# Kernel optimization log

Hardware: AMD Instinct MI355X
Metric: run time of the kernel (lower is better)

The kernel has to match this reference:

```python
import jax, jax.numpy as jnp
import numpy as np

B, T, C = 4, 2048, 768
H, D = 6, 128


def apply_rotary_emb(x, cos, sin):
    # x: (B, T, H, D); cos, sin: (1, T, 1, D//2)
    d = x.shape[-1] // 2
    x1, x2 = x[..., :d], x[..., d:]
    y1 = x1 * cos + x2 * sin
    y2 = -x1 * sin + x2 * cos
    return jnp.concatenate([y1, y2], axis=-1)


def rmsnorm(x):
    eps = 1e-15
    ms = jnp.mean(x * x, axis=-1, keepdims=True)
    return x / jnp.sqrt(ms + eps)


def setup_inputs() -> dict:
    key = jax.random.key(0)
    ks = jax.random.split(key, 7)
    s = 0.02
    return {
        "x": jax.random.normal(ks[0], (B, T, C), jnp.float32),
        "cos": jax.random.normal(ks[1], (1, T, 1, D // 2), jnp.float32),
        "sin": jax.random.normal(ks[2], (1, T, 1, D // 2), jnp.float32),
        "Wq": jax.random.normal(ks[3], (C, C), jnp.float32) * s,
        "Wk": jax.random.normal(ks[4], (C, C), jnp.float32) * s,
        "Wv": jax.random.normal(ks[5], (C, C), jnp.float32) * s,
        "Wo": jax.random.normal(ks[6], (C, C), jnp.float32) * s,
    }


def reference(x, cos, sin, Wq, Wk, Wv, Wo):
    b, t, c = x.shape
    # QKV projections (nn.Linear: x @ W.T)
    q = (x @ Wq.T).reshape(b, t, H, D)
    k = (x @ Wk.T).reshape(b, t, H, D)
    v = (x @ Wv.T).reshape(b, t, H, D)
    # RoPE then QK-RMSNorm
    q = rmsnorm(apply_rotary_emb(q, cos, sin))
    k = rmsnorm(apply_rotary_emb(k, cos, sin))
    # (B, H, T, D)
    q = q.transpose(0, 2, 1, 3)
    k = k.transpose(0, 2, 1, 3)
    v = v.transpose(0, 2, 1, 3)
    scores = jnp.einsum('bhqd,bhkd->bhqk', q, k) / jnp.sqrt(jnp.float32(D))
    causal = jnp.tril(jnp.ones((t, t), dtype=bool))
    scores = jnp.where(causal[None, None], scores, -jnp.inf)
    attn = jax.nn.softmax(scores, axis=-1)
    out = jnp.einsum('bhqk,bhkd->bhqd', attn, v)
    out = out.transpose(0, 2, 1, 3).reshape(b, t, c)
    return out @ Wo.T
```

## Files before the change

kernel.cpp:

```cpp
#include <hip/hip_runtime.h>

#define T_SEQ 2048
#define NH    6
#define HD    128
#define CDIM  768
#define NQKV  2304
#define MROWS 8192
#define NSLOT 384
#define QSCL  0.12754011021989615f

typedef __attribute__((ext_vector_type(8)))  short bf16x8;
typedef __attribute__((ext_vector_type(4)))  float f32x4;
typedef __attribute__((ext_vector_type(16))) float f32x16;
typedef __attribute__((ext_vector_type(2)))  int   i32x2;

__device__ __forceinline__ unsigned short f2bf(float f){
  unsigned int u = __builtin_bit_cast(unsigned int, f);
  u += 0x7fffu + ((u >> 16) & 1u);
  return (unsigned short)(u >> 16);
}
__device__ __forceinline__ float bf2f(unsigned short h){
  unsigned int u = ((unsigned int)h) << 16;
  return __builtin_bit_cast(float, u);
}
__device__ __forceinline__ float ex2(float x){
  return __builtin_amdgcn_exp2f(x);
}
__device__ __forceinline__ unsigned int cvtpk(float lo, float hi){
  unsigned int r;
  asm("v_cvt_pk_bf16_f32 %0, %1, %2" : "=v"(r) : "v"(lo), "v"(hi));
  return r;
}

__device__ __forceinline__ void gload_lds16(const void* g, void* l){
  __builtin_amdgcn_global_load_lds(
      (const __attribute__((address_space(1))) unsigned int*)g,
      (__attribute__((address_space(3))) unsigned int*)l, 16, 0, 0);
}

__device__ __forceinline__ int ncq(int Q){
  return Q < 8 ? 1 : 2;
}
__device__ __forceinline__ int cumc(int Q){
  return Q < 8 ? Q : 8 + 2*(Q-8);
}

__global__ __launch_bounds__(256) void cvt_all(
    const float* __restrict__ x,
    const float* __restrict__ w0, const float* __restrict__ w1,
    const float* __restrict__ w2, const float* __restrict__ w3,
    unsigned short* __restrict__ xb, unsigned short* __restrict__ wout){
  const int bid = blockIdx.x;
  const float* src;
  unsigned short* dst;
  int i;
  if (bid < 6144){
    src = x; dst = xb;
    i = bid * 256 + threadIdx.x;
  } else {
    const int wb = bid - 6144;
    const int which = wb / 576;
    src = which == 0 ? w0 : which == 1 ? w1 : which == 2 ? w2 : w3;
    dst = wout + (size_t)which * CDIM * CDIM;
    i = (wb % 576) * 256 + threadIdx.x;
  }
  float4 v = reinterpret_cast<const float4*>(src)[i];
  ushort4 o;
  o.x = f2bf(v.x); o.y = f2bf(v.y); o.z = f2bf(v.z); o.w = f2bf(v.w);
  reinterpret_cast<ushort4*>(dst)[i] = o;
}

template<int EPI>
__global__ __launch_bounds__(256) void gemm_bt(
    const unsigned short* __restrict__ A,
    const unsigned short* __restrict__ B,
    void* __restrict__ Cv, int M, int N, int K,
    const float* __restrict__ cosp, const float* __restrict__ sinp,
    unsigned short* __restrict__ Vt)
{
  __shared__ unsigned short sh[128 * 128];
  unsigned short* As = sh;
  unsigned short* Bs = sh + 128 * 64;
  const int tid  = threadIdx.x;
  const int lane = tid & 63;
  const int wave = tid >> 6;
  const int lr = lane & 15, lg = lane >> 4;
  const int srow = lane >> 3;
  const int sslot = (lane & 7) ^ (lane >> 3);
  const int gx = gridDim.x, gy = gridDim.y, nwg = gx * gy;
  const int flat = blockIdx.y * gx + blockIdx.x;
  const int nf = (flat & 7) * (nwg >> 3) + (flat >> 3);
  const int row0 = (nf / gy) * 128, col0 = (nf % gy) * 128;
  const int wrow = wave * 32;

  f32x4 acc[2][8];
  const f32x4 z = {0.f, 0.f, 0.f, 0.f};
  #pragma unroll
  for (int i = 0; i < 2; ++i)
    #pragma unroll
    for (int j = 0; j < 8; ++j) acc[i][j] = z;

  for (int k0 = 0; k0 < K; k0 += 64){
    #pragma unroll
    for (int i = 0; i < 4; ++i){
      int seg = wave * 4 + i;
      int r = seg * 8 + srow;
      gload_lds16(&A[(size_t)(row0 + r) * K + k0 + sslot * 8], &As[seg * 512]);
      gload_lds16(&B[(size_t)(col0 + r) * K + k0 + sslot * 8], &Bs[seg * 512]);
    }
    __syncthreads();
    #pragma unroll
    for (int kk = 0; kk < 64; kk += 32){
      bf16x8 af[2], bfr[8];
      #pragma unroll
      for (int mi = 0; mi < 2; ++mi)
        af[mi] = *reinterpret_cast<const bf16x8*>(
            &As[(wrow + mi*16 + lr) * 64 + ((((kk>>3) + lg) ^ (lr & 7)) * 8)]);
      #pragma unroll
      for (int ni = 0; ni < 8; ++ni)
        bfr[ni] = *reinterpret_cast<const bf16x8*>(
            &Bs[(ni*16 + lr) * 64 + ((((kk>>3) + lg) ^ (lr & 7)) * 8)]);
      #pragma unroll
      for (int mi = 0; mi < 2; ++mi)
        #pragma unroll
        for (int ni = 0; ni < 8; ++ni)
          acc[mi][ni] = __builtin_amdgcn_mfma_f32_16x16x32_bf16(af[mi], bfr[ni], acc[mi][ni], 0, 0, 0);
    }
    __syncthreads();
  }

  if (EPI == 0){
    float* Cf = reinterpret_cast<float*>(Cv);
    #pragma unroll
    for (int mi = 0; mi < 2; ++mi)
      #pragma unroll
      for (int ni = 0; ni < 8; ++ni)
        #pragma unroll
        for (int r = 0; r < 4; ++r)
          Cf[(size_t)(row0 + wrow + mi*16 + lg*4 + r) * N + col0 + ni*16 + lr] = acc[mi][ni][r];
  } else {
    unsigned short* Cb = reinterpret_cast<unsigned short*>(Cv);
    const int ct = col0 >> 7;
    if (ct >= 12){
      const int hh = ct - 12;
      const int b2 = row0 >> 11, t0 = row0 & (T_SEQ - 1);
      #pragma unroll
      for (int mi = 0; mi < 2; ++mi)
        #pragma unroll
        for (int ni = 0; ni < 8; ++ni)
          #pragma unroll
          for (int r = 0; r < 4; ++r){
            const int trow = wrow + mi*16 + lg*4 + r;
            const int col  = ni*16 + lr;
            sh[trow * 128 + (col ^ ((trow & 7) << 4))] = f2bf(acc[mi][ni][r]);
          }
      __syncthreads();
      const int dd = tid >> 1, tq = (tid & 1) * 64;
      unsigned short* dst =
          Vt + ((size_t)(b2 * NH + hh) * HD + dd) * T_SEQ + t0 + tq;
      #pragma unroll
      for (int j8 = 0; j8 < 8; ++j8){
        union { int4 v; unsigned short u[8]; } w;
        #pragma unroll
        for (int jj = 0; jj < 8; ++jj){
          const int tt = tq + j8 * 8 + jj;
          w.u[jj] = sh[tt * 128 + (dd ^ (jj << 4))];
        }
        *reinterpret_cast<int4*>(&dst[j8 * 8]) = w.v;
      }
    } else {
      const float post = (ct < 6) ? QSCL : 1.0f;
      #pragma unroll
      for (int mi = 0; mi < 2; ++mi){
        #pragma unroll
        for (int r = 0; r < 4; ++r){
          const int row = row0 + wrow + mi*16 + lg*4 + r;
          const int t = row & (T_SEQ - 1);
          float y1[4], y2[4], ssp = 0.f;
          #pragma unroll
          for (int ni = 0; ni < 4; ++ni){
            const int d = ni*16 + lr;
            float c = cosp[t * 64 + d];
            float s = sinp[t * 64 + d];
            float x1 = acc[mi][ni][r], x2 = acc[mi][ni+4][r];
            y1[ni] = x1 * c + x2 * s;
            y2[ni] = x2 * c - x1 * s;
            ssp += y1[ni]*y1[ni] + y2[ni]*y2[ni];
          }
          #pragma unroll
          for (int off = 1; off < 16; off <<= 1) ssp += __shfl_xor(ssp, off);
          const float inv = rsqrtf(ssp * (1.0f / 128.0f) + 1e-15f) * post;
          #pragma unroll
          for (int ni = 0; ni < 4; ++ni){
            const int d = ni*16 + lr;
            Cb[(size_t)row * N + col0 + d]      = f2bf(y1[ni] * inv);
            Cb[(size_t)row * N + col0 + d + 64] = f2bf(y2[ni] * inv);
          }
        }
      }
    }
  }
}

__global__ __launch_bounds__(256) void attn_fwd(
    const unsigned short* __restrict__ QKVb,
    const unsigned short* __restrict__ Vt,
    unsigned short* __restrict__ AO,
    unsigned short* __restrict__ Op, float* __restrict__ Mp, float* __restrict__ Lp)
{
  __shared__ unsigned short Ks[64][136];
  __shared__ unsigned short Vs[128][72];
  const int tid = threadIdx.x;
  const int lane = tid & 63, wave = tid >> 6;
  const int l31 = lane & 31, hi = lane >> 5;

  const int flat = blockIdx.x;
  const int nf = (flat & 7) * 72 + (flat >> 3);
  const int bh = nf / 24;
  const int L = 23 - (nf % 24);
  int Q, c;
  if (L < 8){ Q = L; c = 0; }
  else      { int m = L - 8; Q = 8 + (m >> 1); c = m & 1; }
  const int nc = ncq(Q);
  const int tiles = 2 * Q + 2;
  const int half = tiles >> 1;
  const int tbeg = (nc == 1) ? 0    : c * half;
  const int tend = (nc == 1) ? tiles : tbeg + half;
  const int b = bh / NH, h = bh % NH;
  const int qw = Q * 128 + wave * 32;

  const unsigned short* Qp = QKVb + (size_t)(b * T_SEQ) * NQKV + h * HD;
  const unsigned short* Kp = QKVb + (size_t)(b * T_SEQ) * NQKV + CDIM + h * HD;
  const unsigned short* Vp = Vt + (size_t)bh * HD * T_SEQ;

  const int kr = tid >> 4, kc4 = (tid & 15) * 8;
  const int vr = tid >> 3, vc4 = (tid & 7) * 8;

  bf16x8 qf[8];
  #pragma unroll
  for (int c4 = 0; c4 < 8; ++c4)
    qf[c4] = *reinterpret_cast<const bf16x8*>(
        &Qp[(size_t)(qw + l31) * NQKV + c4 * 16 + hi * 8]);

  f32x16 o[4];
  #pragma unroll
  for (int db = 0; db < 4; ++db)
    #pragma unroll
    for (int r = 0; r < 16; ++r) o[db][r] = 0.f;
  float mrun = -__builtin_inff(), lrun = 0.f;

  int4 gk0, gk1, gk2, gk3, gv0, gv1, gv2, gv3;
  {
    const int kv0 = tbeg * 64;
    gk0 = *reinterpret_cast<const int4*>(&Kp[(size_t)(kv0 + kr)       * NQKV + kc4]);
    gk1 = *reinterpret_cast<const int4*>(&Kp[(size_t)(kv0 + kr + 16)  * NQKV + kc4]);
    gk2 = *reinterpret_cast<const int4*>(&Kp[(size_t)(kv0 + kr + 32)  * NQKV + kc4]);
    gk3 = *reinterpret_cast<const int4*>(&Kp[(size_t)(kv0 + kr + 48)  * NQKV + kc4]);
    gv0 = *reinterpret_cast<const int4*>(&Vp[(size_t)(vr)       * T_SEQ + kv0 + vc4]);
    gv1 = *reinterpret_cast<const int4*>(&Vp[(size_t)(vr + 32)  * T_SEQ + kv0 + vc4]);
    gv2 = *reinterpret_cast<const int4*>(&Vp[(size_t)(vr + 64)  * T_SEQ + kv0 + vc4]);
    gv3 = *reinterpret_cast<const int4*>(&Vp[(size_t)(vr + 96)  * T_SEQ + kv0 + vc4]);
  }

  for (int t = tbeg; t < tend; ++t){
    *reinterpret_cast<int4*>(&Ks[kr][kc4])        = gk0;
    *reinterpret_cast<int4*>(&Ks[kr + 16][kc4])   = gk1;
    *reinterpret_cast<int4*>(&Ks[kr + 32][kc4])   = gk2;
    *reinterpret_cast<int4*>(&Ks[kr + 48][kc4])   = gk3;
    *reinterpret_cast<int4*>(&Vs[vr][vc4])        = gv0;
    *reinterpret_cast<int4*>(&Vs[vr + 32][vc4])   = gv1;
    *reinterpret_cast<int4*>(&Vs[vr + 64][vc4])   = gv2;
    *reinterpret_cast<int4*>(&Vs[vr + 96][vc4])   = gv3;
    __syncthreads();

    if (t + 1 < tend){
      const int kn = (t + 1) * 64;
      gk0 = *reinterpret_cast<const int4*>(&Kp[(size_t)(kn + kr)       * NQKV + kc4]);
      gk1 = *reinterpret_cast<const int4*>(&Kp[(size_t)(kn + kr + 16)  * NQKV + kc4]);
      gk2 = *reinterpret_cast<const int4*>(&Kp[(size_t)(kn + kr + 32)  * NQKV + kc4]);
      gk3 = *reinterpret_cast<const int4*>(&Kp[(size_t)(kn + kr + 48)  * NQKV + kc4]);
      gv0 = *reinterpret_cast<const int4*>(&Vp[(size_t)(vr)       * T_SEQ + kn + vc4]);
      gv1 = *reinterpret_cast<const int4*>(&Vp[(size_t)(vr + 32)  * T_SEQ + kn + vc4]);
      gv2 = *reinterpret_cast<const int4*>(&Vp[(size_t)(vr + 64)  * T_SEQ + kn + vc4]);
      gv3 = *reinterpret_cast<const int4*>(&Vp[(size_t)(vr + 96)  * T_SEQ + kn + vc4]);
    }

    const int kv0 = t * 64;
    if (kv0 <= qw + 31){
      f32x16 s[2];
      #pragma unroll
      for (int r = 0; r < 16; ++r){ s[0][r] = 0.f; s[1][r] = 0.f; }
      __builtin_amdgcn_s_setprio(1);
      #pragma unroll
      for (int c4 = 0; c4 < 8; ++c4){
        bf16x8 k0 = *reinterpret_cast<const bf16x8*>(&Ks[l31][c4 * 16 + hi * 8]);
        bf16x8 k1 = *reinterpret_cast<const bf16x8*>(&Ks[32 + l31][c4 * 16 + hi * 8]);
        s[0] = __builtin_amdgcn_mfma_f32_32x32x16_bf16(k0, qf[c4], s[0], 0, 0, 0);
        s[1] = __builtin_amdgcn_mfma_f32_32x32x16_bf16(k1, qf[c4], s[1], 0, 0, 0);
      }
      __builtin_amdgcn_s_setprio(0);

      const int qg = qw + l31;
      if (kv0 + 63 > qw){
        #pragma unroll
        for (int blk = 0; blk < 2; ++blk)
          #pragma unroll
          for (int r = 0; r < 16; ++r){
            int kg = kv0 + 32 * blk + (r & 3) + 8 * (r >> 2) + 4 * hi;
            s[blk][r] = (kg <= qg) ? s[blk][r] : -__builtin_inff();
          }
      }

      float t8[8];
      #pragma unroll
      for (int blk = 0; blk < 2; ++blk)
        #pragma unroll
        for (int j = 0; j < 4; ++j)
          t8[blk * 4 + j] = fmaxf(fmaxf(s[blk][4*j], s[blk][4*j+1]),
                                  fmaxf(s[blk][4*j+2], s[blk][4*j+3]));
      float pm = fmaxf(fmaxf(fmaxf(t8[0], t8[1]), fmaxf(t8[2], t8[3])),
                       fmaxf(fmaxf(t8[4], t8[5]), fmaxf(t8[6], t8[7])));
      pm = fmaxf(pm, __shfl_xor(pm, 32));

      if (__any(pm > mrun)){
        float mn = fmaxf(mrun, pm);
        float scf = (mrun == -__builtin_inff()) ? 0.f : ex2(mrun - mn);
        mrun = mn; lrun *= scf;
        #pragma unroll
        for (int r = 0; r < 16; ++r){
          float scr = __shfl(scf, (r & 3) + 8 * (r >> 2) + 4 * hi, 32);
          #pragma unroll
          for (int db = 0; db < 4; ++db) o[db][r] *= scr;
        }
      }

      float a8[8];
      #pragma unroll
      for (int blk = 0; blk < 2; ++blk)
        #pragma unroll
        for (int j = 0; j < 4; ++j){
          float p0 = ex2(s[blk][4*j]   - mrun);
          float p1 = ex2(s[blk][4*j+1] - mrun);
          float p2 = ex2(s[blk][4*j+2] - mrun);
          float p3 = ex2(s[blk][4*j+3] - mrun);
          s[blk][4*j] = p0; s[blk][4*j+1] = p1; s[blk][4*j+2] = p2; s[blk][4*j+3] = p3;
          a8[blk * 4 + j] = (p0 + p1) + (p2 + p3);
        }
      float ls = ((a8[0] + a8[1]) + (a8[2] + a8[3])) + ((a8[4] + a8[5]) + (a8[6] + a8[7]));
      lrun += ls + __shfl_xor(ls, 32);

      __builtin_amdgcn_s_setprio(1);
      #pragma unroll
      for (int kc = 0; kc < 4; ++kc){
        const int blk = kc >> 1, base2 = (kc & 1) * 8;
        unsigned int a0 = cvtpk(s[blk][base2+0], s[blk][base2+1]);
        unsigned int b0 = cvtpk(s[blk][base2+4], s[blk][base2+5]);
        unsigned int a1 = cvtpk(s[blk][base2+2], s[blk][base2+3]);
        unsigned int b1 = cvtpk(s[blk][base2+6], s[blk][base2+7]);
        i32x2 sw0 = __builtin_amdgcn_permlane32_swap((int)a0, (int)b0, false, false);
        i32x2 sw1 = __builtin_amdgcn_permlane32_swap((int)a1, (int)b1, false, false);
        union { bf16x8 v; unsigned int u[4]; } pa;
        pa.u[0] = (unsigned int)sw0[0];
        pa.u[1] = (unsigned int)sw1[0];
        pa.u[2] = (unsigned int)sw0[1];
        pa.u[3] = (unsigned int)sw1[1];
        #pragma unroll
        for (int db = 0; db < 4; ++db){
          bf16x8 vf = *reinterpret_cast<const bf16x8*>(
              &Vs[db * 32 + l31][kc * 16 + hi * 8]);
          o[db] = __builtin_amdgcn_mfma_f32_32x32x16_bf16(pa.v, vf, o[db], 0, 0, 0);
        }
      }
      __builtin_amdgcn_s_setprio(0);
    }
    __syncthreads();
  }

  if (nc == 1){
    float inv = 1.0f / lrun;
    #pragma unroll
    for (int r = 0; r < 16; ++r){
      const int crow = (r & 3) + 8 * (r >> 2) + 4 * hi;
      float ir = __shfl(inv, crow, 32);
      #pragma unroll
      for (int db = 0; db < 4; ++db)
        AO[((size_t)b * T_SEQ + qw + crow) * CDIM + h * HD + db * 32 + l31] =
            f2bf(o[db][r] * ir);
    }
  } else {
    const int slot = bh * 16 + 2 * (Q - 8) + c;
    unsigned short* OpW = Op + (size_t)slot * 128 * 128;
    #pragma unroll
    for (int r = 0; r < 16; ++r){
      const int row = wave * 32 + (r & 3) + 8 * (r >> 2) + 4 * hi;
      #pragma unroll
      for (int db = 0; db < 4; ++db)
        OpW[row * 128 + db * 32 + l31] = f2bf(o[db][r]);
    }
    if (hi == 0){
      Mp[(size_t)slot * 128 + wave * 32 + l31] = mrun;
      Lp[(size_t)slot * 128 + wave * 32 + l31] = lrun;
    }
  }
}

__global__ __launch_bounds__(256) void attn_combine(
    const unsigned short* __restrict__ Op, const float* __restrict__ Mp,
    const float* __restrict__ Lp, unsigned short* __restrict__ AO)
{
  const int Q  = 8 + blockIdx.x;
  const int bh = blockIdx.y;
  const int b = bh / NH, h = bh % NH;
  const int slot0 = bh * 16 + 2 * (Q - 8);
  #pragma unroll
  for (int u = 0; u < 16; ++u){
    int unit = threadIdx.x + u * 256;
    int r = unit >> 5, d4 = unit & 31;
    const float m0 = Mp[(size_t)slot0 * 128 + r];
    const float m1 = Mp[(size_t)(slot0 + 1) * 128 + r];
    const float m = fmaxf(m0, m1);
    const float w0 = __builtin_amdgcn_exp2f(m0 - m);
    const float w1 = __builtin_amdgcn_exp2f(m1 - m);
    const float l = w0 * Lp[(size_t)slot0 * 128 + r]
                  + w1 * Lp[(size_t)(slot0 + 1) * 128 + r];
    const ushort4 v0 = *reinterpret_cast<const ushort4*>(
        &Op[((size_t)slot0 * 128 + r) * 128 + d4 * 4]);
    const ushort4 v1 = *reinterpret_cast<const ushort4*>(
        &Op[((size_t)(slot0 + 1) * 128 + r) * 128 + d4 * 4]);
    const float inv = 1.0f / l;
    ushort4 ov;
    ov.x = f2bf((w0 * bf2f(v0.x) + w1 * bf2f(v1.x)) * inv);
    ov.y = f2bf((w0 * bf2f(v0.y) + w1 * bf2f(v1.y)) * inv);
    ov.z = f2bf((w0 * bf2f(v0.z) + w1 * bf2f(v1.z)) * inv);
    ov.w = f2bf((w0 * bf2f(v0.w) + w1 * bf2f(v1.w)) * inv);
    *reinterpret_cast<ushort4*>(
        &AO[((size_t)b * T_SEQ + Q * 128 + r) * CDIM + h * HD + d4 * 4]) = ov;
  }
}

extern "C" void kernel_launch(void* const* d_in, const int* in_sizes, int n_in,
                              void* d_out, int out_size, void* d_ws, size_t ws_size,
                              hipStream_t stream)
{
  (void)in_sizes; (void)n_in; (void)out_size; (void)ws_size;
  const float* x    = (const float*)d_in[0];
  const float* cosp = (const float*)d_in[1];
  const float* sinp = (const float*)d_in[2];
  const float* Wq   = (const float*)d_in[3];
  const float* Wk   = (const float*)d_in[4];
  const float* Wv   = (const float*)d_in[5];
  const float* Wo   = (const float*)d_in[6];
  float* out = (float*)d_out;

  unsigned short* xb    = (unsigned short*)d_ws;
  unsigned short* Wqkvb = xb    + (size_t)MROWS * CDIM;
  unsigned short* Wob   = Wqkvb + (size_t)NQKV * CDIM;
  unsigned short* QKVb  = Wob   + (size_t)CDIM * CDIM;
  unsigned short* Vtb   = QKVb  + (size_t)MROWS * NQKV;
  unsigned short* AO    = Vtb   + (size_t)MROWS * CDIM;
  unsigned short* Op    = AO    + (size_t)MROWS * CDIM;
  float* Mp = (float*)(Op + (size_t)NSLOT * 128 * 128);
  float* Lp = Mp + (size_t)NSLOT * 128;

  cvt_all<<<8448, 256, 0, stream>>>(x, Wq, Wk, Wv, Wo, xb, Wqkvb);

  gemm_bt<1><<<dim3(MROWS / 128, NQKV / 128), 256, 0, stream>>>(
      xb, Wqkvb, QKVb, MROWS, NQKV, CDIM, cosp, sinp, Vtb);
  attn_fwd<<<576, 256, 0, stream>>>(QKVb, Vtb, AO, Op, Mp, Lp);
  attn_combine<<<dim3(8, 24), 256, 0, stream>>>(Op, Mp, Lp, AO);
  gemm_bt<0><<<dim3(MROWS / 128, CDIM / 128), 256, 0, stream>>>(
      AO, Wob, out, MROWS, CDIM, CDIM, nullptr, nullptr, nullptr);
}
```

Before: 176.8 us.

## Stage 128-key K/V tiles per barrier in attention with dynamic LDS

The attention kernel now loads and stages two 64-key K/V tiles (128 keys) into dynamic shared memory per iteration and processes both sub-tiles between barriers. The aim is to halve the number of __syncthreads and global-load rounds per key range and to issue more loads in flight. The split-kernel boundary is moved to an even tile index so each half holds whole 128-key pairs. In exchange LDS use grows to about 68 KB per block and twice as many prefetch registers are live, which may lower occupancy.

```diff
diff --git a/kernel.cpp b/kernel.cpp
--- a/kernel.cpp
+++ b/kernel.cpp
@@ -40,9 +40,6 @@
 
 __device__ __forceinline__ int ncq(int Q){
   return Q < 8 ? 1 : 2;
-}
-__device__ __forceinline__ int cumc(int Q){
-  return Q < 8 ? Q : 8 + 2*(Q-8);
 }
 
 __global__ __launch_bounds__(256) void cvt_all(
@@ -208,8 +205,9 @@
     unsigned short* __restrict__ AO,
     unsigned short* __restrict__ Op, float* __restrict__ Mp, float* __restrict__ Lp)
 {
-  __shared__ unsigned short Ks[64][136];
-  __shared__ unsigned short Vs[128][72];
+  extern __shared__ unsigned short shm[];
+  unsigned short* Ks = shm;
+  unsigned short* Vs = shm + 128 * 136;
   const int tid = threadIdx.x;
   const int lane = tid & 63, wave = tid >> 6;
   const int l31 = lane & 31, hi = lane >> 5;
@@ -223,9 +221,13 @@
   else      { int m = L - 8; Q = 8 + (m >> 1); c = m & 1; }
   const int nc = ncq(Q);
   const int tiles = 2 * Q + 2;
-  const int half = tiles >> 1;
-  const int tbeg = (nc == 1) ? 0    : c * half;
-  const int tend = (nc == 1) ? tiles : tbeg + half;
+  int tbeg, tend;
+  if (nc == 1){ tbeg = 0; tend = tiles; }
+  else {
+    const int half0 = ((Q + 2) >> 1) << 1;
+    tbeg = c ? half0 : 0;
+    tend = c ? tiles : half0;
+  }
   const int b = bh / NH, h = bh % NH;
   const int qw = Q * 128 + wave * 32;
 
@@ -249,52 +251,67 @@
     for (int r = 0; r < 16; ++r) o[db][r] = 0.f;
   float mrun = -__builtin_inff(), lrun = 0.f;
 
-  int4 gk0, gk1, gk2, gk3, gv0, gv1, gv2, gv3;
-  {
-    const int kv0 = tbeg * 64;
-    gk0 = *reinterpret_cast<const int4*>(&Kp[(size_t)(kv0 + kr)       * NQKV + kc4]);
-    gk1 = *reinterpret_cast<const int4*>(&Kp[(size_t)(kv0 + kr + 16)  * NQKV + kc4]);
-    gk2 = *reinterpret_cast<const int4*>(&Kp[(size_t)(kv0 + kr + 32)  * NQKV + kc4]);
-    gk3 = *reinterpret_cast<const int4*>(&Kp[(size_t)(kv0 + kr + 48)  * NQKV + kc4]);
-    gv0 = *reinterpret_cast<const int4*>(&Vp[(size_t)(vr)       * T_SEQ + kv0 + vc4]);
-    gv1 = *reinterpret_cast<const int4*>(&Vp[(size_t)(vr + 32)  * T_SEQ + kv0 + vc4]);
-    gv2 = *reinterpret_cast<const int4*>(&Vp[(size_t)(vr + 64)  * T_SEQ + kv0 + vc4]);
-    gv3 = *reinterpret_cast<const int4*>(&Vp[(size_t)(vr + 96)  * T_SEQ + kv0 + vc4]);
-  }
-
-  for (int t = tbeg; t < tend; ++t){
-    *reinterpret_cast<int4*>(&Ks[kr][kc4])        = gk0;
-    *reinterpret_cast<int4*>(&Ks[kr + 16][kc4])   = gk1;
-    *reinterpret_cast<int4*>(&Ks[kr + 32][kc4])   = gk2;
-    *reinterpret_cast<int4*>(&Ks[kr + 48][kc4])   = gk3;
-    *reinterpret_cast<int4*>(&Vs[vr][vc4])        = gv0;
-    *reinterpret_cast<int4*>(&Vs[vr + 32][vc4])   = gv1;
-    *reinterpret_cast<int4*>(&Vs[vr + 64][vc4])   = gv2;
-    *reinterpret_cast<int4*>(&Vs[vr + 96][vc4])   = gv3;
+  int4 gk0, gk1, gk2, gk3, gk4, gk5, gk6, gk7;
+  int4 gv0, gv1, gv2, gv3, gv4, gv5, gv6, gv7;
+
+#define LOADST(KV0)                                                            \
+  { const int _k = (KV0);                                                      \
+    gk0 = *reinterpret_cast<const int4*>(&Kp[(size_t)(_k + kr)        * NQKV + kc4]); \
+    gk1 = *reinterpret_cast<const int4*>(&Kp[(size_t)(_k + kr + 16)   * NQKV + kc4]); \
+    gk2 = *reinterpret_cast<const int4*>(&Kp[(size_t)(_k + kr + 32)   * NQKV + kc4]); \
+    gk3 = *reinterpret_cast<const int4*>(&Kp[(size_t)(_k + kr + 48)   * NQKV + kc4]); \
+    gk4 = *reinterpret_cast<const int4*>(&Kp[(size_t)(_k + kr + 64)   * NQKV + kc4]); \
+    gk5 = *reinterpret_cast<const int4*>(&Kp[(size_t)(_k + kr + 80)   * NQKV + kc4]); \
+    gk6 = *reinterpret_cast<const int4*>(&Kp[(size_t)(_k + kr + 96)   * NQKV + kc4]); \
+    gk7 = *reinterpret_cast<const int4*>(&Kp[(size_t)(_k + kr + 112)  * NQKV + kc4]); \
+    gv0 = *reinterpret_cast<const int4*>(&Vp[(size_t)(vr)       * T_SEQ + _k + vc4]);      \
+    gv1 = *reinterpret_cast<const int4*>(&Vp[(size_t)(vr + 32)  * T_SEQ + _k + vc4]);      \
+    gv2 = *reinterpret_cast<const int4*>(&Vp[(size_t)(vr + 64)  * T_SEQ + _k + vc4]);      \
+    gv3 = *reinterpret_cast<const int4*>(&Vp[(size_t)(vr + 96)  * T_SEQ + _k + vc4]);      \
+    gv4 = *reinterpret_cast<const int4*>(&Vp[(size_t)(vr)       * T_SEQ + _k + 64 + vc4]); \
+    gv5 = *reinterpret_cast<const int4*>(&Vp[(size_t)(vr + 32)  * T_SEQ + _k + 64 + vc4]); \
+    gv6 = *reinterpret_cast<const int4*>(&Vp[(size_t)(vr + 64)  * T_SEQ + _k + 64 + vc4]); \
+    gv7 = *reinterpret_cast<const int4*>(&Vp[(size_t)(vr + 96)  * T_SEQ + _k + 64 + vc4]); }
+
+  LOADST(tbeg * 64);
+
+  for (int t = tbeg; t < tend; t += 2){
+    *reinterpret_cast<int4*>(&Ks[(kr)       * 136 + kc4]) = gk0;
+    *reinterpret_cast<int4*>(&Ks[(kr + 16)  * 136 + kc4]) = gk1;
+    *reinterpret_cast<int4*>(&Ks[(kr + 32)  * 136 + kc4]) = gk2;
+    *reinterpret_cast<int4*>(&Ks[(kr + 48)  * 136 + kc4]) = gk3;
+    *reinterpret_cast<int4*>(&Ks[(kr + 64)  * 136 + kc4]) = gk4;
+    *reinterpret_cast<int4*>(&Ks[(kr + 80)  * 136 + kc4]) = gk5;
+    *reinterpret_cast<int4*>(&Ks[(kr + 96)  * 136 + kc4]) = gk6;
+    *reinterpret_cast<int4*>(&Ks[(kr + 112) * 136 + kc4]) = gk7;
+    *reinterpret_cast<int4*>(&Vs[(vr)      * 136 + vc4])      = gv0;
+    *reinterpret_cast<int4*>(&Vs[(vr + 32) * 136 + vc4])      = gv1;
+    *reinterpret_cast<int4*>(&Vs[(vr + 64) * 136 + vc4])      = gv2;
+    *reinterpret_cast<int4*>(&Vs[(vr + 96) * 136 + vc4])      = gv3;
+    *reinterpret_cast<int4*>(&Vs[(vr)      * 136 + 64 + vc4]) = gv4;
+    *reinterpret_cast<int4*>(&Vs[(vr + 32) * 136 + 64 + vc4]) = gv5;
+    *reinterpret_cast<int4*>(&Vs[(vr + 64) * 136 + 64 + vc4]) = gv6;
+    *reinterpret_cast<int4*>(&Vs[(vr + 96) * 136 + 64 + vc4]) = gv7;
     __syncthreads();
 
-    if (t + 1 < tend){
-      const int kn = (t + 1) * 64;
-      gk0 = *reinterpret_cast<const int4*>(&Kp[(size_t)(kn + kr)       * NQKV + kc4]);
-      gk1 = *reinterpret_cast<const int4*>(&Kp[(size_t)(kn + kr + 16)  * NQKV + kc4]);
-      gk2 = *reinterpret_cast<const int4*>(&Kp[(size_t)(kn + kr + 32)  * NQKV + kc4]);
-      gk3 = *reinterpret_cast<const int4*>(&Kp[(size_t)(kn + kr + 48)  * NQKV + kc4]);
-      gv0 = *reinterpret_cast<const int4*>(&Vp[(size_t)(vr)       * T_SEQ + kn + vc4]);
-      gv1 = *reinterpret_cast<const int4*>(&Vp[(size_t)(vr + 32)  * T_SEQ + kn + vc4]);
-      gv2 = *reinterpret_cast<const int4*>(&Vp[(size_t)(vr + 64)  * T_SEQ + kn + vc4]);
-      gv3 = *reinterpret_cast<const int4*>(&Vp[(size_t)(vr + 96)  * T_SEQ + kn + vc4]);
-    }
-
-    const int kv0 = t * 64;
-    if (kv0 <= qw + 31){
+    if (t + 2 < tend) LOADST((t + 2) * 64);
+
+    #pragma unroll
+    for (int sub = 0; sub < 2; ++sub){
+      const int kv0 = (t + sub) * 64;
+      if (kv0 > qw + 31) break;
+      const int rb = sub * 64;
+
       f32x16 s[2];
       #pragma unroll
       for (int r = 0; r < 16; ++r){ s[0][r] = 0.f; s[1][r] = 0.f; }
       __builtin_amdgcn_s_setprio(1);
       #pragma unroll
       for (int c4 = 0; c4 < 8; ++c4){
-        bf16x8 k0 = *reinterpret_cast<const bf16x8*>(&Ks[l31][c4 * 16 + hi * 8]);
-        bf16x8 k1 = *reinterpret_cast<const bf16x8*>(&Ks[32 + l31][c4 * 16 + hi * 8]);
+        bf16x8 k0 = *reinterpret_cast<const bf16x8*>(
+            &Ks[(rb + l31) * 136 + c4 * 16 + hi * 8]);
+        bf16x8 k1 = *reinterpret_cast<const bf16x8*>(
+            &Ks[(rb + 32 + l31) * 136 + c4 * 16 + hi * 8]);
         s[0] = __builtin_amdgcn_mfma_f32_32x32x16_bf16(k0, qf[c4], s[0], 0, 0, 0);
         s[1] = __builtin_amdgcn_mfma_f32_32x32x16_bf16(k1, qf[c4], s[1], 0, 0, 0);
       }
@@ -367,7 +384,7 @@
         #pragma unroll
         for (int db = 0; db < 4; ++db){
           bf16x8 vf = *reinterpret_cast<const bf16x8*>(
-              &Vs[db * 32 + l31][kc * 16 + hi * 8]);
+              &Vs[(db * 32 + l31) * 136 + rb + kc * 16 + hi * 8]);
           o[db] = __builtin_amdgcn_mfma_f32_32x32x16_bf16(pa.v, vf, o[db], 0, 0, 0);
         }
       }
@@ -462,11 +479,14 @@
   float* Mp = (float*)(Op + (size_t)NSLOT * 128 * 128);
   float* Lp = Mp + (size_t)NSLOT * 128;
 
+  (void)hipFuncSetAttribute((const void*)attn_fwd,
+                            hipFuncAttributeMaxDynamicSharedMemorySize, 69632);
+
   cvt_all<<<8448, 256, 0, stream>>>(x, Wq, Wk, Wv, Wo, xb, Wqkvb);
 
   gemm_bt<1><<<dim3(MROWS / 128, NQKV / 128), 256, 0, stream>>>(
       xb, Wqkvb, QKVb, MROWS, NQKV, CDIM, cosp, sinp, Vtb);
-  attn_fwd<<<576, 256, 0, stream>>>(QKVb, Vtb, AO, Op, Mp, Lp);
+  attn_fwd<<<576, 256, 69632, stream>>>(QKVb, Vtb, AO, Op, Mp, Lp);
   attn_combine<<<dim3(8, 24), 256, 0, stream>>>(Op, Mp, Lp, AO);
   gemm_bt<0><<<dim3(MROWS / 128, CDIM / 128), 256, 0, stream>>>(
       AO, Wob, out, MROWS, CDIM, CDIM, nullptr, nullptr, nullptr);
```

Result: no change. 177.3 us (+0.3%).
